# Kernel tuning notes

Hardware: AMD Instinct MI355X
Metric: run time of the kernel (lower is better)

## Reference

```python
import jax, jax.numpy as jnp
import numpy as np

B, N, M, K = 8, 24000, 6000, 32
C_IN, C_MID, C_OUT = 64, 128, 256  # channels=[64,128,256]; conv input is C_IN+3 (dp_fj)


def setup_inputs() -> dict:
    key = jax.random.key(0)
    ks = jax.random.split(key, 8)
    return {
        "query_xyz": jax.random.normal(ks[0], (B, M, 3), jnp.float32),
        "support_xyz": jax.random.normal(ks[1], (B, N, 3), jnp.float32),
        "features": jax.random.normal(ks[2], (B, C_IN, N), jnp.float32),
        "neighbor_idx": jax.random.randint(ks[3], (B, M, K), 0, N, dtype=jnp.int32),
        "W1": jax.random.normal(ks[4], (C_MID, C_IN + 3), jnp.float32) * 0.05,
        "b1": jnp.zeros((C_MID,), jnp.float32),
        "W2": jax.random.normal(ks[5], (C_OUT, C_MID), jnp.float32) * 0.05,
        "b2": jnp.zeros((C_OUT,), jnp.float32),
    }


def _conv1d_relu(x, W, b):
    # pointwise conv1d (kernel size 1) + bias + ReLU; x: [B, Cin, N]
    return jax.nn.relu(jnp.einsum('oc,bcn->bon', W, x) + b[None, :, None])


def reference(query_xyz, support_xyz, features, neighbor_idx, W1, b1, W2, b2):
    # Delayed aggregation: transform features FIRST (convs on support points),
    # then gather neighbors per query and max-reduce.
    x = jnp.concatenate([features, support_xyz.transpose(0, 2, 1)], axis=1)  # [B, C_IN+3, N]
    x = _conv1d_relu(x, W1, b1)   # [B, C_MID, N]
    x = _conv1d_relu(x, W2, b2)   # [B, C_OUT, N]
    # grouper: gather neighbor features fj = x[b, :, neighbor_idx[b, m, k]] -> [B, C_OUT, M, K]
    idx = jnp.broadcast_to(neighbor_idx.reshape(B, 1, M * K), (B, C_OUT, M * K))
    fj = jnp.take_along_axis(x, idx, axis=2).reshape(B, C_OUT, M, K)
    # reduction_layer: max over neighbor dim
    return jnp.max(fj, axis=-1)  # [B, C_OUT, M]
```

## Files before the change

kernel.cpp:

```cpp
#include <hip/hip_runtime.h>

typedef unsigned short u16;
typedef short s16x8 __attribute__((ext_vector_type(8)));
typedef float f32x4 __attribute__((ext_vector_type(4)));

#define B_   8
#define N_   24000
#define M_   6000
#define K_   32
#define CIN  64
#define CMID 128
#define COUT 256
#define KP1  96

__device__ __align__(16) u16 g_W1f[CMID * KP1];
__device__ __align__(16) u16 g_W2f[COUT * CMID];
__device__ __align__(16) u16 g_Yf[(size_t)B_ * N_ * COUT];

__device__ __forceinline__ float bf2f(u16 u) {
    return __uint_as_float(((unsigned)u) << 16);
}
__device__ __forceinline__ u16 f2bf(float f) {
    unsigned u = __float_as_uint(f);
    u += 0x7FFFu + ((u >> 16) & 1u);
    return (u16)(u >> 16);
}

__global__ void prep_weights(const float* __restrict__ W1,
                             const float* __restrict__ W2) {
    int t = blockIdx.x * 256 + threadIdx.x;
    if (t < CMID * KP1) {
        int blk = t >> 9, off = t & 511;
        int L = off >> 3, j = off & 7;
        int ln = L & 15, quad = L >> 4;
        int w = blk / 6, r = blk % 6;
        int k0i = r >> 1, mt = r & 1;
        int row = w * 32 + mt * 16 + ln;
        int col = k0i * 32 + quad * 8 + j;
        g_W1f[t] = (col < 67) ? f2bf(W1[row * 67 + col]) : (u16)0;
    } else {
        int i = t - CMID * KP1;
        int blk = i >> 9, off = i & 511;
        int L = off >> 3, j = off & 7;
        int ln = L & 15, quad = L >> 4;
        int w = blk >> 4, r = blk & 15;
        int k0i = r >> 2, mt = r & 3;
        int row = w * 64 + mt * 16 + ln;
        int col = k0i * 32 + quad * 8 + j;
        g_W2f[i] = f2bf(W2[row * 128 + col]);
    }
}

__global__ __launch_bounds__(256) void conv_fused(
        const float* __restrict__ feat, const float* __restrict__ xyz,
        const float* __restrict__ b1,  const float* __restrict__ b2) {
    __shared__ __align__(16) u16 sm[16896];
    u16* Xs = sm;
    u16* Hs = sm + 6656;
    u16* Ys = sm;

    const int tid  = threadIdx.x;
    const int b    = blockIdx.y;
    const int n0   = blockIdx.x * 64;
    const int w    = tid >> 6;
    const int L    = tid & 63;
    const int ln   = L & 15;
    const int quad = L >> 4;

    if (tid < 64) {
        uint4 z; z.x = z.y = z.z = z.w = 0u;
        u16* xr = Xs + tid * 104;
        *(uint4*)(xr + 64) = z; *(uint4*)(xr + 72) = z;
        *(uint4*)(xr + 80) = z; *(uint4*)(xr + 88) = z;
        const float* s = xyz + (size_t)(b * N_ + n0 + tid) * 3;
        xr[64] = f2bf(s[0]); xr[65] = f2bf(s[1]); xr[66] = f2bf(s[2]);
    }
#pragma unroll
    for (int it = 0; it < 4; ++it) {
        int idx = it * 256 + tid;
        int c   = idx >> 4;
        int p0  = (idx & 15) << 2;
        float4 v = *(const float4*)(feat + (size_t)(b * CIN + c) * N_ + n0 + p0);
        u16* dst = Xs + p0 * 104 + c;
        dst[0]   = f2bf(v.x);
        dst[104] = f2bf(v.y);
        dst[208] = f2bf(v.z);
        dst[312] = f2bf(v.w);
    }
    __syncthreads();

    f32x4 acc1[2][4];
#pragma unroll
    for (int mt = 0; mt < 2; ++mt)
#pragma unroll
        for (int nt = 0; nt < 4; ++nt) {
            f32x4 zz = {0.f, 0.f, 0.f, 0.f};
            acc1[mt][nt] = zz;
        }
#pragma unroll
    for (int k0i = 0; k0i < 3; ++k0i) {
        s16x8 af[2], xf[4];
#pragma unroll
        for (int mt = 0; mt < 2; ++mt)
            af[mt] = *(const s16x8*)(g_W1f + (((w * 3 + k0i) * 2 + mt) << 9) + L * 8);
#pragma unroll
        for (int nt = 0; nt < 4; ++nt)
            xf[nt] = *(const s16x8*)(Xs + (nt * 16 + ln) * 104 + k0i * 32 + quad * 8);
#pragma unroll
        for (int mt = 0; mt < 2; ++mt)
#pragma unroll
            for (int nt = 0; nt < 4; ++nt)
                acc1[mt][nt] = __builtin_amdgcn_mfma_f32_16x16x32_bf16(
                    af[mt], xf[nt], acc1[mt][nt], 0, 0, 0);
    }
#pragma unroll
    for (int mt = 0; mt < 2; ++mt) {
        int m0 = w * 32 + mt * 16 + quad * 4;
        float4 bv = *(const float4*)(b1 + m0);
#pragma unroll
        for (int nt = 0; nt < 4; ++nt) {
            int p = nt * 16 + ln;
            float x0 = acc1[mt][nt][0] + bv.x;
            float x1 = acc1[mt][nt][1] + bv.y;
            float x2 = acc1[mt][nt][2] + bv.z;
            float x3 = acc1[mt][nt][3] + bv.w;
            ushort4 hv;
            hv.x = f2bf(x0 > 0.f ? x0 : 0.f);
            hv.y = f2bf(x1 > 0.f ? x1 : 0.f);
            hv.z = f2bf(x2 > 0.f ? x2 : 0.f);
            hv.w = f2bf(x3 > 0.f ? x3 : 0.f);
            *(ushort4*)(Hs + p * 136 + m0) = hv;
        }
    }
    __syncthreads();

    f32x4 acc2[4][4];
#pragma unroll
    for (int mt = 0; mt < 4; ++mt)
#pragma unroll
        for (int nt = 0; nt < 4; ++nt) {
            f32x4 zz = {0.f, 0.f, 0.f, 0.f};
            acc2[mt][nt] = zz;
        }
#pragma unroll
    for (int k0i = 0; k0i < 4; ++k0i) {
        s16x8 af[4], hf[4];
#pragma unroll
        for (int mt = 0; mt < 4; ++mt)
            af[mt] = *(const s16x8*)(g_W2f + (((w * 4 + k0i) * 4 + mt) << 9) + L * 8);
#pragma unroll
        for (int nt = 0; nt < 4; ++nt)
            hf[nt] = *(const s16x8*)(Hs + (nt * 16 + ln) * 136 + k0i * 32 + quad * 8);
#pragma unroll
        for (int mt = 0; mt < 4; ++mt)
#pragma unroll
            for (int nt = 0; nt < 4; ++nt)
                acc2[mt][nt] = __builtin_amdgcn_mfma_f32_16x16x32_bf16(
                    af[mt], hf[nt], acc2[mt][nt], 0, 0, 0);
    }
    __syncthreads();

#pragma unroll
    for (int mt = 0; mt < 4; ++mt) {
        int c0 = w * 64 + mt * 16 + quad * 4;
        float4 bv = *(const float4*)(b2 + c0);
#pragma unroll
        for (int nt = 0; nt < 4; ++nt) {
            int p = nt * 16 + ln;
            float x0 = acc2[mt][nt][0] + bv.x;
            float x1 = acc2[mt][nt][1] + bv.y;
            float x2 = acc2[mt][nt][2] + bv.z;
            float x3 = acc2[mt][nt][3] + bv.w;
            ushort4 yv;
            yv.x = f2bf(x0 > 0.f ? x0 : 0.f);
            yv.y = f2bf(x1 > 0.f ? x1 : 0.f);
            yv.z = f2bf(x2 > 0.f ? x2 : 0.f);
            yv.w = f2bf(x3 > 0.f ? x3 : 0.f);
            *(ushort4*)(Ys + p * 264 + c0) = yv;
        }
    }
    __syncthreads();

    u16* dstY = g_Yf + ((size_t)b * N_ + n0) * COUT;
#pragma unroll
    for (int i = 0; i < 8; ++i) {
        int g = i * 256 + tid;
        int p = g >> 5, c16 = g & 31;
        *(uint4*)(dstY + (size_t)p * COUT + c16 * 8) =
            *(const uint4*)(Ys + p * 264 + c16 * 8);
    }
}

__global__ __launch_bounds__(256) void gather_max(
        const int* __restrict__ nbr, float* __restrict__ out) {
    __shared__ __align__(16) int sidx[32 * K_];
    __shared__ __align__(16) u16 ymax[COUT * 36];

    const int tid = threadIdx.x;
    const int b   = blockIdx.y;
    const int m0  = blockIdx.x * 32;

    if (m0 + (tid >> 3) < M_)
        *(int4*)(sidx + tid * 4) =
            *(const int4*)(nbr + ((size_t)b * M_ + m0) * K_ + tid * 4);
    __syncthreads();

    const int w = tid >> 6, L = tid & 63;
    const u16* base = g_Yf + (size_t)b * N_ * COUT + L * 4;
#pragma unroll
    for (int i = 0; i < 8; ++i) {
        int ml = w * 8 + i;
        if (m0 + ml >= M_) break;
        ushort4 mx; mx.x = 0; mx.y = 0; mx.z = 0; mx.w = 0;
#pragma unroll
        for (int k = 0; k < K_; ++k) {
            int idx = __builtin_amdgcn_readfirstlane(sidx[ml * K_ + k]);
            idx = ((unsigned)idx < (unsigned)N_) ? idx : 0;
            ushort4 v = *(const ushort4*)(base + (size_t)idx * COUT);
            mx.x = v.x > mx.x ? v.x : mx.x;
            mx.y = v.y > mx.y ? v.y : mx.y;
            mx.z = v.z > mx.z ? v.z : mx.z;
            mx.w = v.w > mx.w ? v.w : mx.w;
        }
        u16* yp = ymax + (L * 4) * 36 + ml;
        yp[0] = mx.x; yp[36] = mx.y; yp[72] = mx.z; yp[108] = mx.w;
    }
    __syncthreads();

    int valid = M_ - m0; if (valid > 32) valid = 32;
#pragma unroll
    for (int i = 0; i < 8; ++i) {
        int c  = i * 32 + (tid >> 3);
        int mc = (tid & 7) << 2;
        if (mc + 4 <= valid) {
            const u16* src = ymax + c * 36 + mc;
            float4 v;
            v.x = bf2f(src[0]); v.y = bf2f(src[1]);
            v.z = bf2f(src[2]); v.w = bf2f(src[3]);
            *(float4*)(out + (size_t)(b * COUT + c) * M_ + m0 + mc) = v;
        }
    }
}

extern "C" void kernel_launch(void* const* d_in, const int* in_sizes, int n_in,
                              void* d_out, int out_size, void* d_ws, size_t ws_size,
                              hipStream_t stream) {
    const float* xyz  = (const float*)d_in[1];
    const float* feat = (const float*)d_in[2];
    const int*   nbr  = (const int*)d_in[3];
    const float* W1   = (const float*)d_in[4];
    const float* b1   = (const float*)d_in[5];
    const float* W2   = (const float*)d_in[6];
    const float* b2   = (const float*)d_in[7];
    float* out = (float*)d_out;
    (void)d_ws; (void)ws_size;

    prep_weights<<<176, 256, 0, stream>>>(W1, W2);
    conv_fused<<<dim3(N_ / 64, B_), 256, 0, stream>>>(feat, xyz, b1, b2);
    gather_max<<<dim3((M_ + 31) / 32, B_), 256, 0, stream>>>(nbr, out);
}
```

Before: 282.8 us.

## Split gather-max by channel quarters with XCD-aware block mapping and wide loads

The gather-max kernel now gives each block a 64-channel quarter of one batch, and maps block IDs so that the blocks on a given XCD share one (batch, quarter) slice of the intermediate feature map, which should improve L2 locality. Each lane loads 16-byte vectors for 8 channels across 4 neighbors in parallel, then reduces over neighbors with xor-shuffles. This replaces 32 serial 8-byte loads per query. The cost is four times as many blocks, each re-reading its neighbor indices, plus extra shuffle work. The design also assumes blocks are dispatched to XCDs round-robin.

```diff
diff --git a/kernel.cpp b/kernel.cpp
--- a/kernel.cpp
+++ b/kernel.cpp
@@ -3,6 +3,7 @@
 typedef unsigned short u16;
 typedef short s16x8 __attribute__((ext_vector_type(8)));
 typedef float f32x4 __attribute__((ext_vector_type(4)));
+typedef unsigned short u16x8 __attribute__((ext_vector_type(8)));
 
 #define B_   8
 #define N_   24000
@@ -12,6 +13,7 @@
 #define CMID 128
 #define COUT 256
 #define KP1  96
+#define QB_  188
 
 __device__ __align__(16) u16 g_W1f[CMID * KP1];
 __device__ __align__(16) u16 g_W2f[COUT * CMID];
@@ -194,50 +196,76 @@
 __global__ __launch_bounds__(256) void gather_max(
         const int* __restrict__ nbr, float* __restrict__ out) {
     __shared__ __align__(16) int sidx[32 * K_];
-    __shared__ __align__(16) u16 ymax[COUT * 36];
+    __shared__ __align__(16) u16 ymax[32 * 400];
 
     const int tid = threadIdx.x;
-    const int b   = blockIdx.y;
-    const int m0  = blockIdx.x * 32;
+    const int l   = blockIdx.x;
+    const int xcd = l & 7;
+    const int j   = l >> 3;
+    const int cw  = j / QB_;
+    const int qb  = j % QB_;
+    const int combo = cw * 8 + xcd;
+    const int b   = combo >> 2;
+    const int q   = combo & 3;
+    const int m0  = qb * 32;
 
     if (m0 + (tid >> 3) < M_)
         *(int4*)(sidx + tid * 4) =
             *(const int4*)(nbr + ((size_t)b * M_ + m0) * K_ + tid * 4);
     __syncthreads();
 
-    const int w = tid >> 6, L = tid & 63;
-    const u16* base = g_Yf + (size_t)b * N_ * COUT + L * 4;
+    const int w  = tid >> 6;
+    const int L  = tid & 63;
+    const int kg = L >> 3;
+    const int co = L & 7;
+    const u16* base = g_Yf + (size_t)b * N_ * COUT + q * 64 + co * 8;
+
 #pragma unroll
     for (int i = 0; i < 8; ++i) {
         int ml = w * 8 + i;
-        if (m0 + ml >= M_) break;
-        ushort4 mx; mx.x = 0; mx.y = 0; mx.z = 0; mx.w = 0;
-#pragma unroll
-        for (int k = 0; k < K_; ++k) {
-            int idx = __builtin_amdgcn_readfirstlane(sidx[ml * K_ + k]);
-            idx = ((unsigned)idx < (unsigned)N_) ? idx : 0;
-            ushort4 v = *(const ushort4*)(base + (size_t)idx * COUT);
-            mx.x = v.x > mx.x ? v.x : mx.x;
-            mx.y = v.y > mx.y ? v.y : mx.y;
-            mx.z = v.z > mx.z ? v.z : mx.z;
-            mx.w = v.w > mx.w ? v.w : mx.w;
-        }
-        u16* yp = ymax + (L * 4) * 36 + ml;
-        yp[0] = mx.x; yp[36] = mx.y; yp[72] = mx.z; yp[108] = mx.w;
+        if (m0 + ml < M_) {
+            int id[4];
+#pragma unroll
+            for (int r = 0; r < 4; ++r)
+                id[r] = sidx[ml * K_ + r * 8 + kg];
+            u16x8 v[4];
+#pragma unroll
+            for (int r = 0; r < 4; ++r) {
+                unsigned u = (unsigned)id[r];
+                u = u < (unsigned)N_ ? u : 0u;
+                v[r] = *(const u16x8*)(base + (size_t)u * COUT);
+            }
+            u16x8 mx = __builtin_elementwise_max(
+                __builtin_elementwise_max(v[0], v[1]),
+                __builtin_elementwise_max(v[2], v[3]));
+
+#pragma unroll
+            for (int mask = 8; mask <= 32; mask <<= 1) {
+                int4 t = *(int4*)&mx;
+                t.x = __shfl_xor(t.x, mask);
+                t.y = __shfl_xor(t.y, mask);
+                t.z = __shfl_xor(t.z, mask);
+                t.w = __shfl_xor(t.w, mask);
+                mx = __builtin_elementwise_max(mx, *(u16x8*)&t);
+            }
+            if (kg == 0)
+                *(u16x8*)(ymax + ml * 400 + co * 8) = mx;
+        }
     }
     __syncthreads();
 
     int valid = M_ - m0; if (valid > 32) valid = 32;
 #pragma unroll
-    for (int i = 0; i < 8; ++i) {
-        int c  = i * 32 + (tid >> 3);
+    for (int it = 0; it < 2; ++it) {
+        int c  = it * 32 + (tid >> 3);
         int mc = (tid & 7) << 2;
         if (mc + 4 <= valid) {
-            const u16* src = ymax + c * 36 + mc;
             float4 v;
-            v.x = bf2f(src[0]); v.y = bf2f(src[1]);
-            v.z = bf2f(src[2]); v.w = bf2f(src[3]);
-            *(float4*)(out + (size_t)(b * COUT + c) * M_ + m0 + mc) = v;
+            v.x = bf2f(ymax[(mc + 0) * 400 + c]);
+            v.y = bf2f(ymax[(mc + 1) * 400 + c]);
+            v.z = bf2f(ymax[(mc + 2) * 400 + c]);
+            v.w = bf2f(ymax[(mc + 3) * 400 + c]);
+            *(float4*)(out + (size_t)(b * COUT + q * 64 + c) * M_ + m0 + mc) = v;
         }
     }
 }
@@ -257,5 +285,5 @@
 
     prep_weights<<<176, 256, 0, stream>>>(W1, W2);
     conv_fused<<<dim3(N_ / 64, B_), 256, 0, stream>>>(feat, xyz, b1, b2);
-    gather_max<<<dim3((M_ + 31) / 32, B_), 256, 0, stream>>>(nbr, out);
-}
+    gather_max<<<32 * QB_, 256, 0, stream>>>(nbr, out);
+}
```

Measured after the change: 267.0 us. 1.06x faster.
